# Performance work log

Measured on AMD Instinct MI355X. Metric: run time of the kernel, lower is better.

The kernel has to match this reference:

```python
import jax, jax.numpy as jnp
import numpy as np

H, DK = 8, 64
INNER = H * DK  # 512


def rel_shift(x):
    # Transformer-XL relative shift (NeMo style): pad left, reshape, drop first row.
    b, h, q, p = x.shape
    x = jnp.pad(x, ((0, 0), (0, 0), (0, 0), (1, 0)))
    x = x.reshape(b, h, p + 1, q)[:, :, 1:]
    return x.reshape(b, h, q, p)


def setup_inputs() -> dict:
    key = jax.random.key(0)
    ks = jax.random.split(key, 16)
    B, T, D = 8, 1024, 512
    s_d = 1.0 / np.sqrt(D)
    s_i = 1.0 / np.sqrt(INNER)
    return {
        "x": jax.random.normal(ks[0], (B, T, D), jnp.float32),
        "pos_emb": jax.random.normal(ks[1], (1, 2 * T - 1, INNER), jnp.float32),
        "w_qkv": jax.random.normal(ks[2], (D, 3 * INNER), jnp.float32) * s_d,
        "w_q": jax.random.normal(ks[3], (INNER, INNER), jnp.float32) * s_i,
        "b_q": jnp.zeros((INNER,), jnp.float32),
        "w_k": jax.random.normal(ks[4], (INNER, INNER), jnp.float32) * s_i,
        "b_k": jnp.zeros((INNER,), jnp.float32),
        "w_v": jax.random.normal(ks[5], (INNER, INNER), jnp.float32) * s_i,
        "b_v": jnp.zeros((INNER,), jnp.float32),
        "w_pos": jax.random.normal(ks[6], (INNER, INNER), jnp.float32) * s_i,
        "bias_u": jax.random.normal(ks[7], (H, DK), jnp.float32) * 0.02,
        "bias_v": jax.random.normal(ks[8], (H, DK), jnp.float32) * 0.02,
        "w_ao": jax.random.normal(ks[9], (INNER, INNER), jnp.float32) * s_i,
        "b_ao": jnp.zeros((INNER,), jnp.float32),
        "w_o": jax.random.normal(ks[10], (INNER, D), jnp.float32) * s_i,
        "b_o": jnp.zeros((D,), jnp.float32),
    }


def reference(x, pos_emb, w_qkv, w_q, b_q, w_k, b_k, w_v, b_v, w_pos,
              bias_u, bias_v, w_ao, b_ao, w_o, b_o):
    B, T, D = x.shape
    # wrapper qkv projection (no bias), then chunk
    q, k, v = jnp.split(x @ w_qkv, 3, axis=-1)
    # RelPositionMultiHeadAttention internal projections
    q = (q @ w_q + b_q).reshape(B, T, H, DK)                       # (b,t,h,d)
    k = (k @ w_k + b_k).reshape(B, T, H, DK).transpose(0, 2, 1, 3)  # (b,h,t,d)
    v = (v @ w_v + b_v).reshape(B, T, H, DK).transpose(0, 2, 1, 3)  # (b,h,t,d)
    p = (pos_emb @ w_pos).reshape(pos_emb.shape[0], -1, H, DK).transpose(0, 2, 1, 3)  # (1,h,2t-1,d)
    q_u = (q + bias_u).transpose(0, 2, 1, 3)  # (b,h,t,d)
    q_v = (q + bias_v).transpose(0, 2, 1, 3)
    matrix_ac = jnp.einsum('bhqd,bhkd->bhqk', q_u, k)      # (b,h,t,t)
    matrix_bd = jnp.einsum('bhqd,xhpd->bhqp', q_v, p)      # (b,h,t,2t-1)
    matrix_bd = rel_shift(matrix_bd)[..., :T]
    scores = (matrix_ac + matrix_bd) * (1.0 / np.sqrt(DK))
    attn = jax.nn.softmax(scores, axis=-1)  # mask=None, dropout inactive at eval
    out = jnp.einsum('bhqk,bhkd->bhqd', attn, v)
    out = out.transpose(0, 2, 1, 3).reshape(B, T, INNER)
    out = out @ w_ao + b_ao   # attention linear_out
    return out @ w_o + b_o    # wrapper to_out
```

## Files before the change

kernel.cpp:

```cpp
#include <hip/hip_runtime.h>
#include <hip/hip_bf16.h>
#include <math.h>

#define H_     8
#define DK_    64
#define INNER_ 512
#define B_     8
#define T_     1024
#define D_     512
#define PLEN_  2047
#define BT_    8192

typedef __attribute__((ext_vector_type(8))) short bf16x8;
typedef __attribute__((ext_vector_type(4))) float f32x4;
typedef __attribute__((ext_vector_type(4))) unsigned short u16x4;
typedef __attribute__((ext_vector_type(8))) unsigned short u16x8;

__device__ __forceinline__ unsigned short f2bf(float f) {
    unsigned u = __float_as_uint(f);
    u += 0x7fffu + ((u >> 16) & 1u);
    return (unsigned short)(u >> 16);
}
__device__ __forceinline__ float bf2f(unsigned short s) {
    return __uint_as_float(((unsigned)s) << 16);
}
__device__ __forceinline__ f32x4 mfma16(bf16x8 a, bf16x8 b, f32x4 c) {
    return __builtin_amdgcn_mfma_f32_16x16x32_bf16(a, b, c, 0, 0, 0);
}
__device__ __forceinline__ void gload16(const unsigned short* g, unsigned short* l) {
    __builtin_amdgcn_global_load_lds(
        (const __attribute__((address_space(1))) void*)g,
        (__attribute__((address_space(3))) void*)l,
        16, 0, 0);
}

#define QSCALE 0.125f

struct SplitA {
    const float* s[4];
    unsigned short* h[4];
    unsigned short* l[4];
    long n[4];
};
__global__ __launch_bounds__(256) void split4(SplitA a)
{
    const int seg = blockIdx.y;
    long i4 = ((long)blockIdx.x * 256 + threadIdx.x) * 4;
    if (i4 >= a.n[seg]) return;
    f32x4 v = *(const f32x4*)(a.s[seg] + i4);
    u16x4 hh, ll;
    #pragma unroll
    for (int i = 0; i < 4; ++i) {
        unsigned short hb = f2bf(v[i]);
        hh[i] = hb;
        ll[i] = f2bf(v[i] - bf2f(hb));
    }
    *(u16x4*)(a.h[seg] + i4) = hh;
    *(u16x4*)(a.l[seg] + i4) = ll;
}

struct PrepW {
    const float* w[5];
    unsigned short* wh[5];
    unsigned short* wl[5];
};
__global__ __launch_bounds__(256) void prep_wb(PrepW p)
{
    const int z = blockIdx.z;
    const float* w = p.w[z];
    unsigned short* wh = p.wh[z];
    unsigned short* wl = p.wl[z];
    __shared__ float sW[32][36];
    const int t = threadIdx.x;
    const int n0 = blockIdx.x * 32, k0 = blockIdx.y * 32;
    {
        int kr = t >> 3, c4 = (t & 7) * 4;
        f32x4 v = *(const f32x4*)(w + (size_t)(k0 + kr) * 512 + n0 + c4);
        #pragma unroll
        for (int i = 0; i < 4; ++i) sW[kr][c4 + i] = v[i];
    }
    __syncthreads();
    {
        int nr = t >> 3, kc = (t & 7) * 4;
        u16x4 hv, lv;
        #pragma unroll
        for (int i = 0; i < 4; ++i) {
            float f = sW[kc + i][nr];
            unsigned short hb = f2bf(f);
            hv[i] = hb;
            lv[i] = f2bf(f - bf2f(hb));
        }
        *(u16x4*)(wh + (size_t)(n0 + nr) * 512 + k0 + kc) = hv;
        *(u16x4*)(wl + (size_t)(n0 + nr) * 512 + k0 + kc) = lv;
    }
}

__global__ __launch_bounds__(256) void misc_k(
    const float* __restrict__ b_ao, const float* __restrict__ w_o,
    const float* __restrict__ b_o, float* __restrict__ be,
    unsigned short* __restrict__ pb_base)
{
    if (blockIdx.x < 2) {
        int n = blockIdx.x * 256 + threadIdx.x;
        float s = b_o[n];
        for (int j = 0; j < 512; ++j) s += b_ao[j] * w_o[(size_t)j * 512 + n];
        be[n] = s;
    } else {
        ((unsigned int*)pb_base)[threadIdx.x] = 0u;
    }
}

template<int MF, bool ALO>
__device__ __forceinline__ void gemm_core(
    f32x4 (&acc)[MF][4],
    const unsigned short* __restrict__ Ah_g,
    const unsigned short* __restrict__ Al_g, int lda,
    const unsigned short* __restrict__ Wh_g,
    const unsigned short* __restrict__ Wl_g,
    int M, int row0, int col0,
    unsigned short* sAh, unsigned short* sAl,
    unsigned short* sWh, unsigned short* sWl)
{
    const int t = threadIdx.x;
    const int lane = t & 63, w = t >> 6;
    const int wm = w >> 1, wn = w & 1;
    const int ln15 = lane & 15, g4 = lane >> 4;
    const int ASZ = MF * 32 * 32;
    const int WSZ = 128 * 32;

    auto stage = [&](int kt, int buf) {
        #pragma unroll
        for (int l = 0; l < MF / 2; ++l) {
            int e = l * 256 + w * 64 + lane;
            int row = e >> 2, slot = e & 3;
            int ss = slot ^ (row & 3);
            int gr = row0 + row;
            if (gr > M - 1) gr = M - 1;
            size_t ga = (size_t)gr * lda + kt * 32 + ss * 8;
            gload16(Ah_g + ga, sAh + buf * ASZ + (l * 256 + w * 64) * 8);
            if constexpr (ALO)
                gload16(Al_g + ga, sAl + buf * ASZ + (l * 256 + w * 64) * 8);
        }
        #pragma unroll
        for (int l = 0; l < 2; ++l) {
            int e = l * 256 + w * 64 + lane;
            int row = e >> 2, slot = e & 3;
            int ss = slot ^ (row & 3);
            size_t gw = (size_t)(col0 + row) * 512 + kt * 32 + ss * 8;
            gload16(Wh_g + gw, sWh + buf * WSZ + (l * 256 + w * 64) * 8);
            gload16(Wl_g + gw, sWl + buf * WSZ + (l * 256 + w * 64) * 8);
        }
    };
    auto comp = [&](int buf) {
        bf16x8 fah[MF], fal[MF], fwh[4], fwl[4];
        #pragma unroll
        for (int i = 0; i < MF; ++i) {
            int ar = wm * (MF * 16) + i * 16 + ln15;
            int sa = (g4 ^ (ar & 3)) * 8;
            fah[i] = *(const bf16x8*)&sAh[buf * ASZ + ar * 32 + sa];
            if constexpr (ALO)
                fal[i] = *(const bf16x8*)&sAl[buf * ASZ + ar * 32 + sa];
        }
        #pragma unroll
        for (int j = 0; j < 4; ++j) {
            int wr = wn * 64 + j * 16 + ln15;
            int sw = (g4 ^ (wr & 3)) * 8;
            fwh[j] = *(const bf16x8*)&sWh[buf * WSZ + wr * 32 + sw];
            fwl[j] = *(const bf16x8*)&sWl[buf * WSZ + wr * 32 + sw];
        }
        __builtin_amdgcn_s_setprio(1);
        #pragma unroll
        for (int mi = 0; mi < MF; ++mi)
            #pragma unroll
            for (int ni = 0; ni < 4; ++ni) {
                acc[mi][ni] = mfma16(fah[mi], fwh[ni], acc[mi][ni]);
                acc[mi][ni] = mfma16(fah[mi], fwl[ni], acc[mi][ni]);
                if constexpr (ALO)
                    acc[mi][ni] = mfma16(fal[mi], fwh[ni], acc[mi][ni]);
            }
        __builtin_amdgcn_s_setprio(0);
    };

    stage(0, 0);
    __syncthreads();
    for (int k2 = 0; k2 < 8; ++k2) {
        stage(2 * k2 + 1, 1);
        comp(0);
        __syncthreads();
        if (k2 < 7) stage(2 * k2 + 2, 0);
        comp(1);
        __syncthreads();
    }
}

#define GEMM_LDS3(MF) \
    __shared__ __align__(16) unsigned short sAh[2][MF * 32 * 32]; \
    __shared__ __align__(16) unsigned short sAl[2][MF * 32 * 32]; \
    __shared__ __align__(16) unsigned short sWh[2][128 * 32];     \
    __shared__ __align__(16) unsigned short sWl[2][128 * 32];
#define GEMM_LDS2(MF) \
    __shared__ __align__(16) unsigned short sAh[2][MF * 32 * 32]; \
    __shared__ __align__(16) unsigned short sWh[2][128 * 32];     \
    __shared__ __align__(16) unsigned short sWl[2][128 * 32];

__global__ __launch_bounds__(256, 3) void gemm_qkv(
    const unsigned short* __restrict__ Ah_g,
    const unsigned short* __restrict__ Wh_g,
    const unsigned short* __restrict__ Wl_g,
    const float* __restrict__ b_q, const float* __restrict__ bu,
    const float* __restrict__ bv, const float* __restrict__ b_k,
    const float* __restrict__ b_v,
    unsigned short* __restrict__ qu, unsigned short* __restrict__ qv,
    unsigned short* __restrict__ kb, unsigned short* __restrict__ vt)
{
    GEMM_LDS2(4)
    f32x4 acc[4][4];
    #pragma unroll
    for (int i = 0; i < 4; ++i)
        #pragma unroll
        for (int j = 0; j < 4; ++j) acc[i][j] = (f32x4){0.f, 0.f, 0.f, 0.f};
    const int row0 = blockIdx.y * 128, col0 = blockIdx.x * 128;
    gemm_core<4, false>(acc, Ah_g, nullptr, 512, Wh_g, Wl_g, BT_, row0, col0,
                        &sAh[0][0], &sAh[0][0], &sWh[0][0], &sWl[0][0]);

    const int t = threadIdx.x;
    const int lane = t & 63, w = t >> 6;
    const int wm = w >> 1, wn = w & 1;
    const int ln15 = lane & 15, g4 = lane >> 4;
    const int grp = col0 >> 9;

    if (grp == 2) {
        #pragma unroll
        for (int mi = 0; mi < 4; ++mi) {
            int gr0 = row0 + wm * 64 + mi * 16 + g4 * 4;
            int bb = gr0 >> 10, t0 = gr0 & 1023;
            #pragma unroll
            for (int ni = 0; ni < 4; ++ni) {
                int gcl = (col0 & 511) + wn * 64 + ni * 16 + ln15;
                float bias = b_v[gcl];
                u16x4 vv;
                #pragma unroll
                for (int r4 = 0; r4 < 4; ++r4) vv[r4] = f2bf(acc[mi][ni][r4] + bias);
                *(u16x4*)(vt + ((size_t)(bb * 512 + gcl)) * 1024 + t0) = vv;
            }
        }
    } else {
        #pragma unroll
        for (int mi = 0; mi < 4; ++mi)
            #pragma unroll
            for (int r4 = 0; r4 < 4; ++r4) {
                int gr = row0 + wm * 64 + mi * 16 + g4 * 4 + r4;
                #pragma unroll
                for (int ni = 0; ni < 4; ++ni) {
                    int gcl = (col0 & 511) + wn * 64 + ni * 16 + ln15;
                    float a = acc[mi][ni][r4];
                    if (grp == 0) {
                        float base = a + b_q[gcl];
                        qu[(size_t)gr * 512 + gcl] = f2bf((base + bu[gcl]) * QSCALE);
                        qv[(size_t)gr * 512 + gcl] = f2bf((base + bv[gcl]) * QSCALE);
                    } else {
                        kb[(size_t)gr * 512 + gcl] = f2bf(a + b_k[gcl]);
                    }
                }
            }
    }
}

__global__ __launch_bounds__(256, 3) void gemm_pos(
    const unsigned short* __restrict__ Ah_g,
    const unsigned short* __restrict__ Wh_g,
    const unsigned short* __restrict__ Wl_g,
    unsigned short* __restrict__ pb0)
{
    GEMM_LDS2(4)
    f32x4 acc[4][4];
    #pragma unroll
    for (int i = 0; i < 4; ++i)
        #pragma unroll
        for (int j = 0; j < 4; ++j) acc[i][j] = (f32x4){0.f, 0.f, 0.f, 0.f};
    const int row0 = blockIdx.y * 128, col0 = blockIdx.x * 128;
    gemm_core<4, false>(acc, Ah_g, nullptr, 512, Wh_g, Wl_g, PLEN_, row0, col0,
                        &sAh[0][0], &sAh[0][0], &sWh[0][0], &sWl[0][0]);

    const int t = threadIdx.x;
    const int lane = t & 63, w = t >> 6;
    const int wm = w >> 1, wn = w & 1;
    const int ln15 = lane & 15, g4 = lane >> 4;
    #pragma unroll
    for (int mi = 0; mi < 4; ++mi)
        #pragma unroll
        for (int r4 = 0; r4 < 4; ++r4) {
            int gr = row0 + wm * 64 + mi * 16 + g4 * 4 + r4;
            if (gr >= PLEN_) continue;
            #pragma unroll
            for (int ni = 0; ni < 4; ++ni) {
                int gc = col0 + wn * 64 + ni * 16 + ln15;
                pb0[(size_t)gr * 512 + gc] = f2bf(acc[mi][ni][r4]);
            }
        }
}

struct WeffA {
    const unsigned short* ah[4];
    const unsigned short* al[4];
    int lda[4];
    const unsigned short* wh[4];
    const unsigned short* wl[4];
    float* c[4];
};
__global__ __launch_bounds__(256, 3) void gemm_weff(WeffA a)
{
    GEMM_LDS3(2)
    const int z = blockIdx.z;
    f32x4 acc[2][4];
    #pragma unroll
    for (int i = 0; i < 2; ++i)
        #pragma unroll
        for (int j = 0; j < 4; ++j) acc[i][j] = (f32x4){0.f, 0.f, 0.f, 0.f};
    const int row0 = blockIdx.y * 64, col0 = blockIdx.x * 128;
    gemm_core<2, true>(acc, a.ah[z], a.al[z], a.lda[z], a.wh[z], a.wl[z],
                       512, row0, col0,
                       &sAh[0][0], &sAl[0][0], &sWh[0][0], &sWl[0][0]);

    const int t = threadIdx.x;
    const int lane = t & 63, w = t >> 6;
    const int wm = w >> 1, wn = w & 1;
    const int ln15 = lane & 15, g4 = lane >> 4;
    float* C = a.c[z];
    #pragma unroll
    for (int mi = 0; mi < 2; ++mi)
        #pragma unroll
        for (int r4 = 0; r4 < 4; ++r4) {
            int gr = row0 + wm * 32 + mi * 16 + g4 * 4 + r4;
            #pragma unroll
            for (int ni = 0; ni < 4; ++ni) {
                int gc = col0 + wn * 64 + ni * 16 + ln15;
                C[(size_t)gr * 512 + gc] = acc[mi][ni][r4];
            }
        }
}

__global__ __launch_bounds__(256, 3) void gemm_out(
    const unsigned short* __restrict__ Ah_g,
    const unsigned short* __restrict__ Al_g,
    const unsigned short* __restrict__ Wh_g,
    const unsigned short* __restrict__ Wl_g,
    const float* __restrict__ beff, float* __restrict__ C)
{
    GEMM_LDS3(2)
    f32x4 acc[2][4];
    #pragma unroll
    for (int i = 0; i < 2; ++i)
        #pragma unroll
        for (int j = 0; j < 4; ++j) acc[i][j] = (f32x4){0.f, 0.f, 0.f, 0.f};
    const int row0 = blockIdx.y * 64, col0 = blockIdx.x * 128;
    gemm_core<2, true>(acc, Ah_g, Al_g, 512, Wh_g, Wl_g, BT_, row0, col0,
                       &sAh[0][0], &sAl[0][0], &sWh[0][0], &sWl[0][0]);

    const int t = threadIdx.x;
    const int lane = t & 63, w = t >> 6;
    const int wm = w >> 1, wn = w & 1;
    const int ln15 = lane & 15, g4 = lane >> 4;
    #pragma unroll
    for (int mi = 0; mi < 2; ++mi)
        #pragma unroll
        for (int r4 = 0; r4 < 4; ++r4) {
            int gr = row0 + wm * 32 + mi * 16 + g4 * 4 + r4;
            #pragma unroll
            for (int ni = 0; ni < 4; ++ni) {
                int gc = col0 + wn * 64 + ni * 16 + ln15;
                C[(size_t)gr * 512 + gc] = acc[mi][ni][r4] + beff[gc];
            }
        }
}

__global__ __launch_bounds__(256, 2) void attn_v8(
    const unsigned short* __restrict__ qu_g,
    const unsigned short* __restrict__ qv_g,
    const unsigned short* __restrict__ kb_g,
    const unsigned short* __restrict__ vt_g,
    const unsigned short* __restrict__ pb_g,
    unsigned short* __restrict__ atth,
    unsigned short* __restrict__ attl)
{
    __shared__ __align__(16) unsigned short sK[2][64 * 64];
    __shared__ __align__(16) unsigned short sP[2][64 * 64];
    __shared__ __align__(16) unsigned short sV[2][64 * 64];
    __shared__ __align__(16) unsigned short ringb[64][132];
    __shared__ __align__(16) unsigned short sProb[64][72];

    const int t = threadIdx.x;
    const int lane = t & 63, w = t >> 6;
    const int ln15 = lane & 15, g4 = lane >> 4;

    const int wg = blockIdx.x;
    const int idx = (wg & 7) * 128 + (wg >> 3);
    const int q0 = (idx & 15) * 64;
    const int bh = idx >> 4;
    const int h = bh & 7, b = bh >> 3;
    const size_t tok0 = (size_t)b * T_;
    const int hd = h * DK_;
    const int qq = w * 16 + ln15;

    auto stage_chunk = [&](int c, int buf) {
        #pragma unroll
        for (int l = 0; l < 2; ++l) {
            int e = l * 256 + w * 64 + lane;
            int row = e >> 3, slot = e & 7;
            int sl = slot ^ (row & 7);
            int lofs = buf * 4096 + (l * 256 + w * 64) * 8;
            gload16(kb_g + (tok0 + c * 64 + row) * INNER_ + hd + sl * 8, &sK[0][lofs]);
            gload16(vt_g + ((size_t)(b * H_ + h) * DK_ + row) * T_ + c * 64 + sl * 8, &sV[0][lofs]);
            long p = (long)(c * 64 - q0 + 1023 + row);
            gload16(pb_g + p * INNER_ + hd + sl * 8, &sP[0][lofs]);
        }
    };

    #pragma unroll
    for (int l = 0; l < 2; ++l) {
        int e = l * 256 + w * 64 + lane;
        int row = e >> 3, slot = e & 7;
        int sl = slot ^ (row & 7);
        size_t src = (tok0 + q0 + row) * INNER_ + hd + sl * 8;
        gload16(qu_g + src, &sK[0][(l * 256 + w * 64) * 8]);
        gload16(qv_g + src, &sP[0][(l * 256 + w * 64) * 8]);
    }
    __syncthreads();
    bf16x8 fqu[2], fqv[2];
    #pragma unroll
    for (int ki = 0; ki < 2; ++ki) {
        int sl = (ki * 4 + g4) ^ (qq & 7);
        fqu[ki] = *(const bf16x8*)&sK[0][qq * 64 + sl * 8];
        fqv[ki] = *(const bf16x8*)&sP[0][qq * 64 + sl * 8];
    }
    __syncthreads();

    #pragma unroll
    for (int l = 0; l < 2; ++l) {
        int e = l * 256 + w * 64 + lane;
        int row = e >> 3, slot = e & 7;
        int sl = slot ^ (row & 7);
        long p = (long)(959 - q0 + row);
        gload16(pb_g + p * INNER_ + hd + sl * 8, &sP[0][4096 + (l * 256 + w * 64) * 8]);
    }
    stage_chunk(0, 0);
    __syncthreads();

    #pragma unroll
    for (int n = 0; n < 4; ++n) {
        f32x4 bdv = {0.f, 0.f, 0.f, 0.f};
        #pragma unroll
        for (int ki = 0; ki < 2; ++ki) {
            int prow = n * 16 + ln15;
            int sl = (ki * 4 + g4) ^ (prow & 7);
            bf16x8 pf = *(const bf16x8*)&sP[0][4096 + prow * 64 + sl * 8];
            bdv = mfma16(pf, fqv[ki], bdv);
        }
        #pragma unroll
        for (int r4 = 0; r4 < 4; ++r4)
            ringb[qq][(n * 16 + g4 * 4 + r4 + qq) & 127] = f2bf(bdv[r4]);
    }
    __syncthreads();

    float m = -1e30f, den = 0.f;
    f32x4 o[4];
    #pragma unroll
    for (int i = 0; i < 4; ++i) o[i] = (f32x4){0.f, 0.f, 0.f, 0.f};

    auto compute_chunk = [&](int c, int buf) {
        const int bofs = buf * 4096;
        f32x4 sc[4], bd[4];
        #pragma unroll
        for (int n = 0; n < 4; ++n) {
            sc[n] = (f32x4){0.f, 0.f, 0.f, 0.f};
            bd[n] = (f32x4){0.f, 0.f, 0.f, 0.f};
        }
        __builtin_amdgcn_s_setprio(1);
        #pragma unroll
        for (int ki = 0; ki < 2; ++ki)
            #pragma unroll
            for (int n = 0; n < 4; ++n) {
                int krow = n * 16 + ln15;
                int sl = (ki * 4 + g4) ^ (krow & 7);
                bf16x8 kf = *(const bf16x8*)&sK[0][bofs + krow * 64 + sl * 8];
                sc[n] = mfma16(kf, fqu[ki], sc[n]);
                bf16x8 pf = *(const bf16x8*)&sP[0][bofs + krow * 64 + sl * 8];
                bd[n] = mfma16(pf, fqv[ki], bd[n]);
            }
        __builtin_amdgcn_s_setprio(0);

        const int pbase = (c & 1) ? 0 : 64;
        #pragma unroll
        for (int n = 0; n < 4; ++n)
            #pragma unroll
            for (int r4 = 0; r4 < 4; ++r4)
                ringb[qq][(pbase + n * 16 + g4 * 4 + r4 + qq) & 127] = f2bf(bd[n][r4]);

        float s[4][4];
        float mx = -1e30f;
        #pragma unroll
        for (int n = 0; n < 4; ++n) {
            const int st2 = (c * 64 + 64 + n * 16 + g4 * 4) & 127;
            u16x4 rv = *(const u16x4*)&ringb[qq][st2];
            #pragma unroll
            for (int r4 = 0; r4 < 4; ++r4) {
                float v = sc[n][r4] + bf2f(rv[r4]);
                s[n][r4] = v;
                mx = fmaxf(mx, v);
            }
        }
        mx = fmaxf(mx, __shfl_xor(mx, 16));
        mx = fmaxf(mx, __shfl_xor(mx, 32));
        float newm = fmaxf(m, mx);
        float scale = __expf(m - newm);
        m = newm;
        float ls = 0.f;
        #pragma unroll
        for (int n = 0; n < 4; ++n) {
            u16x4 pv4;
            #pragma unroll
            for (int r4 = 0; r4 < 4; ++r4) {
                float p = __expf(s[n][r4] - newm);
                ls += p;
                pv4[r4] = f2bf(p);
            }
            *(u16x4*)&sProb[qq][n * 16 + g4 * 4] = pv4;
        }
        ls += __shfl_xor(ls, 16);
        ls += __shfl_xor(ls, 32);
        den = den * scale + ls;
        #pragma unroll
        for (int n2 = 0; n2 < 4; ++n2) {
            o[n2][0] *= scale; o[n2][1] *= scale;
            o[n2][2] *= scale; o[n2][3] *= scale;
        }

        __builtin_amdgcn_s_setprio(1);
        #pragma unroll
        for (int ki = 0; ki < 2; ++ki) {
            bf16x8 pa = *(const bf16x8*)&sProb[qq][ki * 32 + g4 * 8];
            #pragma unroll
            for (int n2 = 0; n2 < 4; ++n2) {
                int drow = n2 * 16 + ln15;
                int sl = (ki * 4 + g4) ^ (drow & 7);
                bf16x8 vf = *(const bf16x8*)&sV[0][bofs + drow * 64 + sl * 8];
                o[n2] = mfma16(vf, pa, o[n2]);
            }
        }
        __builtin_amdgcn_s_setprio(0);
    };

    for (int c2 = 0; c2 < 8; ++c2) {
        int c = c2 * 2;
        stage_chunk(c + 1, 1);
        compute_chunk(c, 0);
        __syncthreads();
        if (c2 < 7) stage_chunk(c + 2, 0);
        compute_chunk(c + 1, 1);
        __syncthreads();
    }

    const float inv = 1.0f / den;
    #pragma unroll
    for (int n2 = 0; n2 < 4; ++n2) {
        u16x4 hv, lv;
        #pragma unroll
        for (int r4 = 0; r4 < 4; ++r4) {
            float val = o[n2][r4] * inv;
            unsigned short hb = f2bf(val);
            hv[r4] = hb;
            lv[r4] = f2bf(val - bf2f(hb));
        }
        size_t oidx = (tok0 + q0 + qq) * INNER_ + hd + n2 * 16 + g4 * 4;
        *(u16x4*)(atth + oidx) = hv;
        *(u16x4*)(attl + oidx) = lv;
    }
}

extern "C" void kernel_launch(void* const* d_in, const int* in_sizes, int n_in,
                              void* d_out, int out_size, void* d_ws, size_t ws_size,
                              hipStream_t stream)
{
    const float* x     = (const float*)d_in[0];
    const float* pos   = (const float*)d_in[1];
    const float* w_qkv = (const float*)d_in[2];
    const float* w_q   = (const float*)d_in[3];
    const float* b_q   = (const float*)d_in[4];
    const float* w_k   = (const float*)d_in[5];
    const float* b_k   = (const float*)d_in[6];
    const float* w_v   = (const float*)d_in[7];
    const float* b_v   = (const float*)d_in[8];
    const float* w_pos = (const float*)d_in[9];
    const float* bu    = (const float*)d_in[10];
    const float* bv    = (const float*)d_in[11];
    const float* w_ao  = (const float*)d_in[12];
    const float* b_ao  = (const float*)d_in[13];
    const float* w_o   = (const float*)d_in[14];
    const float* b_o   = (const float*)d_in[15];
    float* out = (float*)d_out;

    unsigned short* u = (unsigned short*)d_ws;
    const size_t SZ = (size_t)BT_ * INNER_;
    unsigned short* xh   = u;
    unsigned short* xl   = xh + SZ;
    unsigned short* qu   = xl + SZ;
    unsigned short* qv   = qu + SZ;
    unsigned short* kb   = qv + SZ;
    unsigned short* vt   = kb + SZ;
    unsigned short* atth = vt + SZ;
    unsigned short* attl = atth + SZ;
    unsigned short* pb_base = attl + SZ;
    unsigned short* pb0  = pb_base + 512;
    unsigned short* posh = pb_base + 1049600;
    unsigned short* posl = posh + 1049600;
    unsigned short* wqkvh = posl + 1049600;
    unsigned short* wqkvl = wqkvh + 786432;
    unsigned short* waoh  = wqkvl + 786432;
    unsigned short* waol  = waoh + 262144;
    unsigned short* w5    = waol + 262144;
    unsigned short* wq_h = w5;              unsigned short* wq_l = w5 + 262144;
    unsigned short* wk_h = w5 + 2*262144;   unsigned short* wk_l = w5 + 3*262144;
    unsigned short* wv_h = w5 + 4*262144;   unsigned short* wv_l = w5 + 5*262144;
    unsigned short* wo_h = w5 + 6*262144;   unsigned short* wo_l = w5 + 7*262144;
    unsigned short* wp_h = w5 + 8*262144;   unsigned short* wp_l = w5 + 9*262144;
    float* weffC = (float*)(w5 + 10*262144);
    unsigned short* wcat_h = (unsigned short*)(weffC + 4*262144);
    unsigned short* wcat_l = wcat_h + 786432;
    unsigned short* woe_h  = wcat_l + 786432;
    unsigned short* woe_l  = woe_h + 262144;
    float* beff = (float*)(woe_l + 262144);

    dim3 blk(256);

    SplitA sa;
    sa.s[0] = x;     sa.h[0] = xh;    sa.l[0] = xl;    sa.n[0] = (long)SZ;
    sa.s[1] = w_qkv; sa.h[1] = wqkvh; sa.l[1] = wqkvl; sa.n[1] = 786432L;
    sa.s[2] = w_ao;  sa.h[2] = waoh;  sa.l[2] = waol;  sa.n[2] = 262144L;
    sa.s[3] = pos;   sa.h[3] = posh;  sa.l[3] = posl;  sa.n[3] = (long)PLEN_ * 512;
    split4<<<dim3(4096, 4), blk, 0, stream>>>(sa);

    PrepW p5;
    p5.w[0] = w_q;   p5.wh[0] = wq_h; p5.wl[0] = wq_l;
    p5.w[1] = w_k;   p5.wh[1] = wk_h; p5.wl[1] = wk_l;
    p5.w[2] = w_v;   p5.wh[2] = wv_h; p5.wl[2] = wv_l;
    p5.w[3] = w_o;   p5.wh[3] = wo_h; p5.wl[3] = wo_l;
    p5.w[4] = w_pos; p5.wh[4] = wp_h; p5.wl[4] = wp_l;
    prep_wb<<<dim3(16, 16, 5), blk, 0, stream>>>(p5);

    WeffA wa;
    wa.ah[0] = wqkvh;        wa.al[0] = wqkvl;        wa.lda[0] = 1536;
    wa.ah[1] = wqkvh + 512;  wa.al[1] = wqkvl + 512;  wa.lda[1] = 1536;
    wa.ah[2] = wqkvh + 1024; wa.al[2] = wqkvl + 1024; wa.lda[2] = 1536;
    wa.ah[3] = waoh;         wa.al[3] = waol;         wa.lda[3] = 512;
    wa.wh[0] = wq_h; wa.wl[0] = wq_l;
    wa.wh[1] = wk_h; wa.wl[1] = wk_l;
    wa.wh[2] = wv_h; wa.wl[2] = wv_l;
    wa.wh[3] = wo_h; wa.wl[3] = wo_l;
    wa.c[0] = weffC;             wa.c[1] = weffC + 262144;
    wa.c[2] = weffC + 2*262144;  wa.c[3] = weffC + 3*262144;
    gemm_weff<<<dim3(4, 8, 4), blk, 0, stream>>>(wa);

    PrepW p4;
    p4.w[0] = weffC;            p4.wh[0] = wcat_h;            p4.wl[0] = wcat_l;
    p4.w[1] = weffC + 262144;   p4.wh[1] = wcat_h + 262144;   p4.wl[1] = wcat_l + 262144;
    p4.w[2] = weffC + 2*262144; p4.wh[2] = wcat_h + 2*262144; p4.wl[2] = wcat_l + 2*262144;
    p4.w[3] = weffC + 3*262144; p4.wh[3] = woe_h;             p4.wl[3] = woe_l;
    p4.w[4] = nullptr; p4.wh[4] = nullptr; p4.wl[4] = nullptr;
    prep_wb<<<dim3(16, 16, 4), blk, 0, stream>>>(p4);

    misc_k<<<3, blk, 0, stream>>>(b_ao, w_o, b_o, beff, pb_base);

    gemm_qkv<<<dim3(12, 64), blk, 0, stream>>>(xh, wcat_h, wcat_l,
        b_q, bu, bv, b_k, b_v, qu, qv, kb, vt);
    gemm_pos<<<dim3(4, 16), blk, 0, stream>>>(posh, wp_h, wp_l, pb0);

    attn_v8<<<1024, blk, 0, stream>>>(qu, qv, kb, vt, pb0, atth, attl);

    gemm_out<<<dim3(4, 128), blk, 0, stream>>>(atth, attl, woe_h, woe_l, beff, out);
}
```

Measured before the change: 193.1 us.

## Replace syncthreads with partial vmcnt waits to keep prefetch loads in flight

Swaps the full __syncthreads barriers in the GEMM core and attention loops for raw s_barrier plus s_waitcnt vmcnt(N). The wait now covers only the older buffer's global-to-LDS loads, so the next stage's prefetch can stay outstanding while compute runs. This is meant to remove the stall where every barrier drained all pending loads. It relies on hand-counted load numbers per stage (6 or 8), which breaks silently if the staging code changes. It also drops one barrier after the ringb writes in the attention kernel, which may create an LDS race.

```diff
diff --git a/kernel.cpp b/kernel.cpp
--- a/kernel.cpp
+++ b/kernel.cpp
@@ -33,6 +33,9 @@
         (__attribute__((address_space(3))) void*)l,
         16, 0, 0);
 }
+#define BARRIER()  __builtin_amdgcn_s_barrier()
+#define SCHEDBAR() __builtin_amdgcn_sched_barrier(0)
+#define VMCNT(N)   asm volatile("s_waitcnt vmcnt(" #N ")" ::: "memory")
 
 #define QSCALE 0.125f
 
@@ -127,6 +130,7 @@
     const int ln15 = lane & 15, g4 = lane >> 4;
     const int ASZ = MF * 32 * 32;
     const int WSZ = 128 * 32;
+    constexpr int NLD = (MF / 2) * (ALO ? 2 : 1) + 4;
 
     auto stage = [&](int kt, int buf) {
         #pragma unroll
@@ -182,14 +186,21 @@
     };
 
     stage(0, 0);
-    __syncthreads();
     for (int k2 = 0; k2 < 8; ++k2) {
+        BARRIER();
         stage(2 * k2 + 1, 1);
+        if constexpr (NLD == 6) { VMCNT(6); } else { VMCNT(8); }
+        BARRIER(); SCHEDBAR();
         comp(0);
-        __syncthreads();
-        if (k2 < 7) stage(2 * k2 + 2, 0);
+        BARRIER();
+        if (k2 < 7) {
+            stage(2 * k2 + 2, 0);
+            if constexpr (NLD == 6) { VMCNT(6); } else { VMCNT(8); }
+        } else {
+            VMCNT(0);
+        }
+        BARRIER(); SCHEDBAR();
         comp(1);
-        __syncthreads();
     }
 }
 
@@ -374,7 +385,7 @@
         }
 }
 
-__global__ __launch_bounds__(256, 2) void attn_v8(
+__global__ __launch_bounds__(256, 2) void attn_v9(
     const unsigned short* __restrict__ qu_g,
     const unsigned short* __restrict__ qv_g,
     const unsigned short* __restrict__ kb_g,
@@ -444,7 +455,8 @@
         gload16(pb_g + p * INNER_ + hd + sl * 8, &sP[0][4096 + (l * 256 + w * 64) * 8]);
     }
     stage_chunk(0, 0);
-    __syncthreads();
+    VMCNT(6);
+    BARRIER(); SCHEDBAR();
 
     #pragma unroll
     for (int n = 0; n < 4; ++n) {
@@ -460,7 +472,6 @@
         for (int r4 = 0; r4 < 4; ++r4)
             ringb[qq][(n * 16 + g4 * 4 + r4 + qq) & 127] = f2bf(bdv[r4]);
     }
-    __syncthreads();
 
     float m = -1e30f, den = 0.f;
     f32x4 o[4];
@@ -551,13 +562,22 @@
     };
 
     for (int c2 = 0; c2 < 8; ++c2) {
-        int c = c2 * 2;
+        const int c = 2 * c2;
+        BARRIER();
         stage_chunk(c + 1, 1);
+        VMCNT(6);
+        BARRIER(); SCHEDBAR();
         compute_chunk(c, 0);
-        __syncthreads();
-        if (c2 < 7) stage_chunk(c + 2, 0);
+
+        BARRIER();
+        if (c2 < 7) {
+            stage_chunk(c + 2, 0);
+            VMCNT(6);
+        } else {
+            VMCNT(0);
+        }
+        BARRIER(); SCHEDBAR();
         compute_chunk(c + 1, 1);
-        __syncthreads();
     }
 
     const float inv = 1.0f / den;
@@ -674,7 +694,7 @@
         b_q, bu, bv, b_k, b_v, qu, qv, kb, vt);
     gemm_pos<<<dim3(4, 16), blk, 0, stream>>>(posh, wp_h, wp_l, pb0);
 
-    attn_v8<<<1024, blk, 0, stream>>>(qu, qv, kb, vt, pb0, atth, attl);
+    attn_v9<<<1024, blk, 0, stream>>>(qu, qv, kb, vt, pb0, atth, attl);
 
     gemm_out<<<dim3(4, 128), blk, 0, stream>>>(atth, attl, woe_h, woe_l, beff, out);
 }
```

Result: no change. 195.5 us (+1.3%).
